# Optimization experiments

Measured on AMD Instinct MI355X. Metric: run time of the kernel, lower is better.

## Reference

```python
import jax, jax.numpy as jnp
import numpy as np

EMBED = 512
HEADS = 8
DIM_HEAD = 64          # embed_dim // 8
LANDMARKS = 256        # embed_dim // 2
PINV_ITERS = 6
RES_K = 33             # nystrom residual_conv_kernel default
SCALE = DIM_HEAD ** -0.5


def layer_norm(x, g, b, eps=1e-5):
    mu = x.mean(-1, keepdims=True)
    var = ((x - mu) ** 2).mean(-1, keepdims=True)
    return (x - mu) / jnp.sqrt(var + eps) * g + b


def moore_penrose_pinv(x, iters=PINV_ITERS):
    # iterative Moore-Penrose pseudo-inverse (lucidrains nystrom-attention)
    ax = jnp.abs(x)
    z = jnp.swapaxes(x, -1, -2) / (ax.sum(-1).max() * ax.sum(-2).max())
    I = jnp.eye(x.shape[-1], dtype=x.dtype)
    for _ in range(iters):
        xz = x @ z
        z = 0.25 * z @ (13. * I - xz @ (15. * I - xz @ (7. * I - xz)))
    return z


def nystrom_attention(x, w_qkv, w_out, b_out, res_k):
    b, n, _ = x.shape
    m = LANDMARKS
    pad = (m - n % m) % m
    xp = jnp.pad(x, ((0, 0), (pad, 0), (0, 0)))  # left-pad like F.pad(..., padding, 0)
    np_ = n + pad
    qkv = (xp @ w_qkv).reshape(b, np_, 3, HEADS, DIM_HEAD)
    q = qkv[:, :, 0].transpose(0, 2, 1, 3) * SCALE   # [b,h,np,dh]
    k = qkv[:, :, 1].transpose(0, 2, 1, 3)
    v = qkv[:, :, 2].transpose(0, 2, 1, 3)
    l = np_ // m
    q_l = q.reshape(b, HEADS, m, l, DIM_HEAD).mean(3)  # [b,h,m,dh]
    k_l = k.reshape(b, HEADS, m, l, DIM_HEAD).mean(3)
    attn1 = jax.nn.softmax(jnp.einsum('bhid,bhjd->bhij', q, k_l), -1)    # [b,h,np,m]
    attn2 = jax.nn.softmax(jnp.einsum('bhid,bhjd->bhij', q_l, k_l), -1)  # [b,h,m,m]
    attn3 = jax.nn.softmax(jnp.einsum('bhid,bhjd->bhij', q_l, k), -1)    # [b,h,m,np]
    out = (attn1 @ moore_penrose_pinv(attn2)) @ (attn3 @ v)              # [b,h,np,dh]
    # depthwise residual conv over the sequence dim, per head (shared across dh)
    v_c = v.transpose(0, 3, 1, 2).reshape(b * DIM_HEAD, HEADS, np_)
    res = jax.lax.conv_general_dilated(
        v_c, res_k[:, None, :], (1,), [(RES_K // 2, RES_K // 2)],
        dimension_numbers=('NCH', 'OIH', 'NCH'), feature_group_count=HEADS)
    out = out + res.reshape(b, DIM_HEAD, HEADS, np_).transpose(0, 2, 3, 1)
    out = out.transpose(0, 2, 1, 3).reshape(b, np_, HEADS * DIM_HEAD)
    out = out @ w_out + b_out
    return out[:, -n:]  # drop left padding


def dwconv2d(x, w, b, k):
    # x: [B,C,H,W], w: [C,1,k,k] depthwise
    y = jax.lax.conv_general_dilated(
        x, w, (1, 1), [(k // 2, k // 2)] * 2,
        dimension_numbers=('NCHW', 'OIHW', 'NCHW'), feature_group_count=x.shape[1])
    return y + b[None, :, None, None]


def ppeg(x, H, W, w7, b7, w5, b5, w3, b3):
    B, _, C = x.shape
    cls_tok, feat = x[:, :1], x[:, 1:]
    f = feat.transpose(0, 2, 1).reshape(B, C, H, W)
    y = f + dwconv2d(f, w7, b7, 7) + dwconv2d(f, w5, b5, 5) + dwconv2d(f, w3, b3, 3)
    y = y.reshape(B, C, H * W).transpose(0, 2, 1)
    return jnp.concatenate([cls_tok, y], axis=1)


def reference(h, w_fc1, b_fc1, cls_token,
              ln1_g, ln1_b, qkv1_w, out1_w, out1_b, res1_k,
              conv7_w, conv7_b, conv5_w, conv5_b, conv3_w, conv3_b,
              ln2_g, ln2_b, qkv2_w, out2_w, out2_b, res2_k,
              lnf_g, lnf_b):
    h = jax.nn.relu(h @ w_fc1 + b_fc1)                 # [B,N,512]
    B, N, C = h.shape
    _H = int(np.ceil(np.sqrt(N)))
    add = _H * _H - N
    h = jnp.concatenate([h, h[:, :add]], axis=1)       # square padding
    h = jnp.concatenate([jnp.broadcast_to(cls_token, (B, 1, C)), h], axis=1)
    h = h + nystrom_attention(layer_norm(h, ln1_g, ln1_b), qkv1_w, out1_w, out1_b, res1_k)
    h = ppeg(h, _H, _H, conv7_w, conv7_b, conv5_w, conv5_b, conv3_w, conv3_b)
    h = h + nystrom_attention(layer_norm(h, ln2_g, ln2_b), qkv2_w, out2_w, out2_b, res2_k)
    return layer_norm(h, lnf_g, lnf_b)[:, 0]           # [B,512]


def setup_inputs() -> dict:
    key = jax.random.key(0)
    ks = jax.random.split(key, 24)
    B, N, IN_DIM = 2, 4096, 1024
    w = lambda k, shape, s=0.02: jax.random.normal(k, shape, jnp.float32) * s
    z = lambda shape: jnp.zeros(shape, jnp.float32)
    o = lambda shape: jnp.ones(shape, jnp.float32)
    return {
        'h': jax.random.normal(ks[0], (B, N, IN_DIM), jnp.float32),
        'w_fc1': w(ks[1], (IN_DIM, EMBED)), 'b_fc1': z((EMBED,)),
        'cls_token': w(ks[2], (1, 1, EMBED)),
        'ln1_g': o((EMBED,)), 'ln1_b': z((EMBED,)),
        'qkv1_w': w(ks[3], (EMBED, 3 * HEADS * DIM_HEAD)),
        'out1_w': w(ks[4], (HEADS * DIM_HEAD, EMBED)), 'out1_b': z((EMBED,)),
        'res1_k': w(ks[5], (HEADS, RES_K), 0.1),
        'conv7_w': w(ks[6], (EMBED, 1, 7, 7), 0.05), 'conv7_b': z((EMBED,)),
        'conv5_w': w(ks[7], (EMBED, 1, 5, 5), 0.05), 'conv5_b': z((EMBED,)),
        'conv3_w': w(ks[8], (EMBED, 1, 3, 3), 0.05), 'conv3_b': z((EMBED,)),
        'ln2_g': o((EMBED,)), 'ln2_b': z((EMBED,)),
        'qkv2_w': w(ks[9], (EMBED, 3 * HEADS * DIM_HEAD)),
        'out2_w': w(ks[10], (HEADS * DIM_HEAD, EMBED)), 'out2_b': z((EMBED,)),
        'res2_k': w(ks[11], (HEADS, RES_K), 0.1),
        'lnf_g': o((EMBED,)), 'lnf_b': z((EMBED,)),
    }
```

## Files before the change

### kernel.cpp

```cpp
#include <hip/hip_runtime.h>
#include <hip/hip_bf16.h>

#define HEADS 8
#define DH 64
#define EMB 512
#define NP 4352
#define NTOK 4097
#define PADF 255
#define LM 256
#define SCALE 0.125f

typedef __attribute__((ext_vector_type(8))) short bf8;
typedef __attribute__((ext_vector_type(4))) float f4;
typedef __attribute__((ext_vector_type(8))) unsigned short us8;
typedef __attribute__((ext_vector_type(4))) unsigned short us4;
typedef unsigned short u16;

__device__ __forceinline__ u16 f2b(float f){
  union { float f; unsigned u; } x; x.f = f;
  unsigned r = x.u + 0x7fffu + ((x.u>>16)&1u);
  return (u16)(r>>16);
}
__device__ __forceinline__ float b2f(u16 h){
  union { unsigned u; float f; } x; x.u = ((unsigned)h)<<16;
  return x.f;
}

__device__ __forceinline__ void gload_lds(const u16* g, u16* l){
  __builtin_amdgcn_global_load_lds((const __attribute__((address_space(1))) void*)g,
                                   (__attribute__((address_space(3))) void*)l, 16, 0, 0);
}

#define WAITCNT(N) asm volatile("s_waitcnt vmcnt(" #N ")" ::: "memory")
#define SCHED_FENCE() __builtin_amdgcn_sched_barrier(0)
#define BARRIER() __builtin_amdgcn_s_barrier()

template<int MODE>
__global__ __launch_bounds__(256)
void k_g128(const u16* __restrict__ A, const u16* __restrict__ B,
            float* __restrict__ C, u16* __restrict__ C16,
            int K, int lda, int ldb, int ldc,
            long sAb, long sAh, long sBb, long sBh, long sCb, long sCh, int nh,
            float alpha, const float* __restrict__ bias, int relu, int rowoff,
            int nx, int ksplit)
{
  int z = blockIdx.z;
  const u16* Ab = A + (long)(z/nh)*sAb + (long)(z%nh)*sAh;
  const u16* Bb = B + (long)(z/nh)*sBb + (long)(z%nh)*sBh;
  long cb = (long)(z/nh)*sCb + (long)(z%nh)*sCh;
  int bx = blockIdx.x % nx, kc = blockIdx.x / nx;
  int m0 = blockIdx.y*128, n0 = bx*128;
  int klen = K/ksplit, kbeg = kc*klen, nch = klen/32;
  __shared__ u16 As[2][4096];
  __shared__ u16 Bs[2][4096];
  int tid=threadIdx.x, w=tid>>6, lane=tid&63, q=lane>>4, lr=lane&15;
  int wrow=(w>>1)*64, wcol=(w&1)*64;
  int srow = tid>>2, scol = (tid&3)*8;
  const u16* ga  = Ab + (long)(m0+srow)*lda + kbeg + scol;
  const u16* ga2 = Ab + (long)(m0+64+srow)*lda + kbeg + scol;
  const u16* gb  = Bb + (long)(n0+srow)*ldb + kbeg + scol;
  const u16* gb2 = Bb + (long)(n0+64+srow)*ldb + kbeg + scol;
  int lo = srow*32 + scol;
  f4 acc[4][4] = {};
  auto stage = [&](int r, int c){
    gload_lds(ga  + c*32, &As[r][lo]);
    gload_lds(ga2 + c*32, &As[r][2048+lo]);
    gload_lds(gb  + c*32, &Bs[r][lo]);
    gload_lds(gb2 + c*32, &Bs[r][2048+lo]);
  };
  auto compute = [&](int r){
    bf8 af[4], bfr[4];
    #pragma unroll
    for(int rr=0;rr<4;rr++) af[rr]  = *(const bf8*)&As[r][(wrow + rr*16 + lr)*32 + q*8];
    #pragma unroll
    for(int t=0;t<4;t++) bfr[t] = *(const bf8*)&Bs[r][(wcol + t*16 + lr)*32 + q*8];
    #pragma unroll
    for(int rr=0;rr<4;rr++)
      #pragma unroll
      for(int t=0;t<4;t++)
        acc[rr][t] = __builtin_amdgcn_mfma_f32_16x16x32_bf16(af[rr], bfr[t], acc[rr][t], 0,0,0);
  };
  stage(0,0);
  stage(1,1);
  for(int c=0;c<nch;c++){
    if(c+1<nch) WAITCNT(4); else WAITCNT(0);
    SCHED_FENCE();
    BARRIER();
    compute(c&1);
    SCHED_FENCE();
    BARRIER();
    SCHED_FENCE();
    if(c+2<nch) stage(c&1, c+2);
  }
  #pragma unroll
  for(int r=0;r<4;r++){
    #pragma unroll
    for(int t=0;t<4;t++){
      #pragma unroll
      for(int e=0;e<4;e++){
        int gm = m0 + wrow + r*16 + q*4 + e;
        int gn = n0 + wcol + t*16 + lr;
        float v = acc[r][t][e]*alpha;
        if(MODE==4){
          if(bias && kc==0) v += bias[gn];
          if(gm>=rowoff) atomicAdd(&C[cb + (long)(gm-rowoff)*ldc + gn], v);
        } else {
          if(bias) v += bias[gn];
          if(relu) v = fmaxf(v,0.f);
          if(MODE==0) C[cb + (long)gm*ldc + gn] = v;
          else if(MODE==2) C16[cb + (long)gm*ldc + gn] = f2b(v);
          else { if(gm>=rowoff) C[cb + (long)(gm-rowoff)*ldc + gn] += v; }
        }
      }
    }
  }
}

template<int MODE>
__global__ __launch_bounds__(256)
void k_g64(const u16* __restrict__ A, const u16* __restrict__ B,
           float* __restrict__ C, u16* __restrict__ C16,
           int K, int lda, int ldb, int ldc,
           long sAb, long sAh, long sBb, long sBh, long sCb, long sCh, int nh,
           float alpha, const float* __restrict__ bias, int rowoff, int moff,
           int nx, int ksplit)
{
  int z = blockIdx.z;
  const u16* Ab = A + (long)(z/nh)*sAb + (long)(z%nh)*sAh;
  const u16* Bb = B + (long)(z/nh)*sBb + (long)(z%nh)*sBh;
  long cb = (long)(z/nh)*sCb + (long)(z%nh)*sCh;
  int bx = blockIdx.x % nx, kc = blockIdx.x / nx;
  int m0 = blockIdx.y*64 + moff, n0 = bx*64;
  int klen = K/ksplit, kbeg = kc*klen, nch = klen/32;
  __shared__ u16 As[2][2048];
  __shared__ u16 Bs[2][2048];
  int tid=threadIdx.x, w=tid>>6, lane=tid&63, q=lane>>4, lr=lane&15;
  int srow = tid>>2, scol = (tid&3)*8;
  const u16* ga = Ab + (long)(m0+srow)*lda + kbeg + scol;
  const u16* gb = Bb + (long)(n0+srow)*ldb + kbeg + scol;
  int lo = srow*32 + scol;
  f4 acc[4] = {};
  auto stage = [&](int r, int c){
    gload_lds(ga + c*32, &As[r][lo]);
    gload_lds(gb + c*32, &Bs[r][lo]);
  };
  auto compute = [&](int r){
    bf8 af = *(const bf8*)&As[r][(w*16 + lr)*32 + q*8];
    #pragma unroll
    for(int t=0;t<4;t++){
      bf8 bfr = *(const bf8*)&Bs[r][(t*16 + lr)*32 + q*8];
      acc[t] = __builtin_amdgcn_mfma_f32_16x16x32_bf16(af, bfr, acc[t], 0,0,0);
    }
  };
  stage(0,0);
  stage(1,1);
  for(int c=0;c<nch;c++){
    if(c+1<nch) WAITCNT(2); else WAITCNT(0);
    SCHED_FENCE();
    BARRIER();
    compute(c&1);
    SCHED_FENCE();
    BARRIER();
    SCHED_FENCE();
    if(c+2<nch) stage(c&1, c+2);
  }
  #pragma unroll
  for(int t=0;t<4;t++){
    #pragma unroll
    for(int e=0;e<4;e++){
      int gm = m0 + w*16 + q*4 + e;
      int gn = n0 + t*16 + lr;
      float v = acc[t][e]*alpha;
      if(MODE==0) C[cb + (long)gm*ldc + gn] = v;
      else if(MODE==2) C16[cb + (long)gm*ldc + gn] = f2b(v);
      else if(MODE==3) atomicAdd(&C[cb + (long)gm*ldc + gn], v);
      else if(MODE==5){
        v += bias[gn];
        if(gm>=rowoff) C[cb + (long)(gm-rowoff)*ldc + gn] += v;
      }
    }
  }
}

__global__ __launch_bounds__(256)
void k_pg3(const u16* __restrict__ Ah, const u16* __restrict__ Al,
           const u16* __restrict__ Bh, const u16* __restrict__ Bl,
           u16* __restrict__ Oh, u16* __restrict__ Ol, float na, float nd,
           u16* __restrict__ TOh, u16* __restrict__ TOl, float ta, float td)
{
  long zo = (long)blockIdx.z*65536;
  int m0 = blockIdx.y*32, n0 = blockIdx.x*64;
  __shared__ u16 S[2][6144];
  int tid=threadIdx.x, w=tid>>6, lane=tid&63, q=lane>>4, lr=lane&15;
  int t2 = tid & 127;
  const u16* srcA = (tid<128 ? Ah : Al) + zo + (long)(m0 + (t2>>2))*256 + (t2&3)*8;
  const u16* srcBh = Bh + zo + (long)(n0 + (tid>>2))*256 + (tid&3)*8;
  const u16* srcBl = Bl + zo + (long)(n0 + (tid>>2))*256 + (tid&3)*8;
  f4 acc[2] = {};
  auto stage = [&](int r, int c){
    gload_lds(srcA  + c*32, &S[r][tid*8]);
    gload_lds(srcBh + c*32, &S[r][2048 + tid*8]);
    gload_lds(srcBl + c*32, &S[r][4096 + tid*8]);
  };
  int mrow = (w>>1)*16 + lr;
  auto compute = [&](int r){
    bf8 ah = *(const bf8*)&S[r][mrow*32 + q*8];
    bf8 al = *(const bf8*)&S[r][1024 + mrow*32 + q*8];
    #pragma unroll
    for(int t=0;t<2;t++){
      int nrow = (w&1)*32 + t*16 + lr;
      bf8 bh = *(const bf8*)&S[r][2048 + nrow*32 + q*8];
      bf8 bl = *(const bf8*)&S[r][4096 + nrow*32 + q*8];
      acc[t] = __builtin_amdgcn_mfma_f32_16x16x32_bf16(ah, bh, acc[t], 0,0,0);
      acc[t] = __builtin_amdgcn_mfma_f32_16x16x32_bf16(ah, bl, acc[t], 0,0,0);
      acc[t] = __builtin_amdgcn_mfma_f32_16x16x32_bf16(al, bh, acc[t], 0,0,0);
    }
  };
  stage(0,0);
  stage(1,1);
  for(int c=0;c<8;c++){
    if(c<7) WAITCNT(3); else WAITCNT(0);
    SCHED_FENCE();
    BARRIER();
    compute(c&1);
    SCHED_FENCE();
    BARRIER();
    SCHED_FENCE();
    if(c+2<8) stage(c&1, c+2);
  }
  #pragma unroll
  for(int t=0;t<2;t++){
    int gn = n0 + (w&1)*32 + t*16 + lr;
    if(Oh){
      #pragma unroll
      for(int r=0;r<4;r++){
        int gm = m0 + (w>>1)*16 + q*4 + r;
        float v = na*acc[t][r] + ((gm==gn)?nd:0.f);
        u16 h = f2b(v);
        long o = zo + (long)gm*256 + gn;
        Oh[o] = h; Ol[o] = f2b(v - b2f(h));
      }
    }
    if(TOh){
      us4 th, tl;
      #pragma unroll
      for(int r=0;r<4;r++){
        int gm = m0 + (w>>1)*16 + q*4 + r;
        float v = ta*acc[t][r] + ((gm==gn)?td:0.f);
        u16 h = f2b(v);
        th[r] = h; tl[r] = f2b(v - b2f(h));
      }
      long o = zo + (long)gn*256 + (m0 + (w>>1)*16 + q*4);
      *(us4*)&TOh[o] = th; *(us4*)&TOl[o] = tl;
    }
  }
}

__global__ __launch_bounds__(256)
void k_pg3b(const u16* __restrict__ Zh, const u16* __restrict__ Zl,
            const u16* __restrict__ Ph, const u16* __restrict__ Pl,
            const u16* __restrict__ Bh, const u16* __restrict__ Bl,
            u16* __restrict__ Ozh, u16* __restrict__ Ozl,
            u16* __restrict__ Oyh, u16* __restrict__ Oyl,
            u16* __restrict__ Tyh, u16* __restrict__ Tyl)
{
  long zo = (long)blockIdx.z*65536;
  int ysel = blockIdx.y>>3;
  int m0 = (blockIdx.y&7)*32, n0 = blockIdx.x*64;
  const u16* Ah = ysel ? Ph : Zh;
  const u16* Al = ysel ? Pl : Zl;
  __shared__ u16 S[2][6144];
  int tid=threadIdx.x, w=tid>>6, lane=tid&63, q=lane>>4, lr=lane&15;
  int t2 = tid & 127;
  const u16* srcA = (tid<128 ? Ah : Al) + zo + (long)(m0 + (t2>>2))*256 + (t2&3)*8;
  const u16* srcBh = Bh + zo + (long)(n0 + (tid>>2))*256 + (tid&3)*8;
  const u16* srcBl = Bl + zo + (long)(n0 + (tid>>2))*256 + (tid&3)*8;
  f4 acc[2] = {};
  auto stage = [&](int r, int c){
    gload_lds(srcA  + c*32, &S[r][tid*8]);
    gload_lds(srcBh + c*32, &S[r][2048 + tid*8]);
    gload_lds(srcBl + c*32, &S[r][4096 + tid*8]);
  };
  int mrow = (w>>1)*16 + lr;
  auto compute = [&](int r){
    bf8 ah = *(const bf8*)&S[r][mrow*32 + q*8];
    bf8 al = *(const bf8*)&S[r][1024 + mrow*32 + q*8];
    #pragma unroll
    for(int t=0;t<2;t++){
      int nrow = (w&1)*32 + t*16 + lr;
      bf8 bh = *(const bf8*)&S[r][2048 + nrow*32 + q*8];
      bf8 bl = *(const bf8*)&S[r][4096 + nrow*32 + q*8];
      acc[t] = __builtin_amdgcn_mfma_f32_16x16x32_bf16(ah, bh, acc[t], 0,0,0);
      acc[t] = __builtin_amdgcn_mfma_f32_16x16x32_bf16(ah, bl, acc[t], 0,0,0);
      acc[t] = __builtin_amdgcn_mfma_f32_16x16x32_bf16(al, bh, acc[t], 0,0,0);
    }
  };
  stage(0,0);
  stage(1,1);
  for(int c=0;c<8;c++){
    if(c<7) WAITCNT(3); else WAITCNT(0);
    SCHED_FENCE();
    BARRIER();
    compute(c&1);
    SCHED_FENCE();
    BARRIER();
    SCHED_FENCE();
    if(c+2<8) stage(c&1, c+2);
  }
  #pragma unroll
  for(int t=0;t<2;t++){
    int gn = n0 + (w&1)*32 + t*16 + lr;
    if(!ysel){
      #pragma unroll
      for(int r=0;r<4;r++){
        int gm = m0 + (w>>1)*16 + q*4 + r;
        float v = 0.25f*acc[t][r];
        u16 h = f2b(v);
        long o = zo + (long)gm*256 + gn;
        Ozh[o] = h; Ozl[o] = f2b(v - b2f(h));
      }
    } else {
      us4 th, tl;
      #pragma unroll
      for(int r=0;r<4;r++){
        int gm = m0 + (w>>1)*16 + q*4 + r;
        float v = 0.25f*acc[t][r];
        u16 h = f2b(v);
        long o = zo + (long)gm*256 + gn;
        Oyh[o] = h; Oyl[o] = f2b(v - b2f(h));
        float tv = -v + ((gm==gn)?7.f:0.f);
        u16 h2 = f2b(tv);
        th[r] = h2; tl[r] = f2b(tv - b2f(h2));
      }
      long o = zo + (long)gn*256 + (m0 + (w>>1)*16 + q*4);
      *(us4*)&Tyh[o] = th; *(us4*)&Tyl[o] = tl;
    }
  }
}

__global__ __launch_bounds__(256)
void k_att3(const u16* __restrict__ qkv16, const u16* __restrict__ ql,
            const u16* __restrict__ vT, float* __restrict__ partO,
            float* __restrict__ pm, float* __restrict__ pl)
{
  int kc = blockIdx.x, jt = blockIdx.y, z = blockIdx.z;
  int b = z>>3, h = z&7;
  __shared__ u16 SQ[64*64];
  __shared__ u16 SK[2][64*64];
  __shared__ u16 SV[2][64*64];
  __shared__ u16 SP[64*64];
  int tid=threadIdx.x, w=tid>>6, lane=tid&63, q=lane>>4, lr=lane&15;
  const u16* kb = qkv16 + (long)b*NP*1536 + 512 + h*64;
  const u16* vb = vT + (long)z*64*NP;
  int t00 = kc*256;
  {
    const u16* qb = ql + (long)z*16384 + jt*64*64;
    #pragma unroll
    for(int p=0;p<2;p++){
      int idx = tid + p*256; int row = idx>>3; int js = ((idx&7)^(row&7))<<3;
      gload_lds(qb + row*64 + js, &SQ[idx*8]);
    }
  }
  auto stageKV = [&](int r, int i){
    int t0 = t00 + i*64;
    #pragma unroll
    for(int p=0;p<2;p++){
      int idx = tid + p*256; int row = idx>>3; int js = ((idx&7)^(row&7))<<3;
      gload_lds(kb + (long)(t0+row)*1536 + js, &SK[r][idx*8]);
      gload_lds(vb + (long)row*NP + t0 + js, &SV[r][idx*8]);
    }
  };
  stageKV(0,0);
  __syncthreads();
  int ar = w*16+lr;
  bf8 af0 = *(const bf8*)&SQ[ar*64 + ((q^(ar&7))<<3)];
  bf8 af1 = *(const bf8*)&SQ[ar*64 + (((q|4)^(ar&7))<<3)];
  f4 o[4] = {};
  float m[4] = {-3e38f,-3e38f,-3e38f,-3e38f};
  float l[4] = {0.f,0.f,0.f,0.f};
  for(int i=0;i<4;i++){
    int cur = i&1;
    if(i<3) stageKV(cur^1, i+1);
    f4 s[4] = {};
    #pragma unroll
    for(int t=0;t<4;t++){
      int br = t*16+lr;
      bf8 b0 = *(const bf8*)&SK[cur][br*64 + ((q^(br&7))<<3)];
      bf8 b1 = *(const bf8*)&SK[cur][br*64 + (((q|4)^(br&7))<<3)];
      s[t] = __builtin_amdgcn_mfma_f32_16x16x32_bf16(af0, b0, s[t], 0,0,0);
      s[t] = __builtin_amdgcn_mfma_f32_16x16x32_bf16(af1, b1, s[t], 0,0,0);
    }
    float tm[4];
    #pragma unroll
    for(int e=0;e<4;e++) tm[e] = fmaxf(fmaxf(s[0][e],s[1][e]), fmaxf(s[2][e],s[3][e]));
    #pragma unroll
    for(int sh=1; sh<16; sh<<=1)
      #pragma unroll
      for(int e=0;e<4;e++) tm[e] = fmaxf(tm[e], __shfl_xor(tm[e], sh));
    float rs[4];
    #pragma unroll
    for(int e=0;e<4;e++){
      float mn = fmaxf(m[e], tm[e]);
      float sc = expf(m[e]-mn);
      m[e] = mn;
      l[e] *= sc;
      rs[e] = 0.f;
      o[0][e]*=sc; o[1][e]*=sc; o[2][e]*=sc; o[3][e]*=sc;
    }
    #pragma unroll
    for(int t=0;t<4;t++)
      #pragma unroll
      for(int e=0;e<4;e++){
        float p = expf(s[t][e]-m[e]);
        rs[e] += p;
        int prow = w*16+q*4+e, pcol = t*16+lr;
        SP[prow*64 + (((pcol>>3)^(prow&7))<<3) + (pcol&7)] = f2b(p);
      }
    #pragma unroll
    for(int sh=1; sh<16; sh<<=1)
      #pragma unroll
      for(int e=0;e<4;e++) rs[e] += __shfl_xor(rs[e], sh);
    #pragma unroll
    for(int e=0;e<4;e++) l[e] += rs[e];
    int pr = w*16+lr;
    #pragma unroll
    for(int ks=0;ks<2;ks++){
      bf8 pa = *(const bf8*)&SP[pr*64 + (((ks*4+q)^(pr&7))<<3)];
      #pragma unroll
      for(int t2=0;t2<4;t2++){
        int rr = t2*16+lr;
        bf8 vv = *(const bf8*)&SV[cur][rr*64 + (((ks*4+q)^(rr&7))<<3)];
        o[t2] = __builtin_amdgcn_mfma_f32_16x16x32_bf16(pa, vv, o[t2], 0,0,0);
      }
    }
    __syncthreads();
  }
  long pb = (long)(z*17+kc)*256 + jt*64 + w*16;
  #pragma unroll
  for(int e=0;e<4;e++){
    int jg = q*4+e;
    #pragma unroll
    for(int t2=0;t2<4;t2++)
      partO[(pb + jg)*64 + t2*16 + lr] = o[t2][e];
    if(lr==0){ pm[pb + jg] = m[e]; pl[pb + jg] = l[e]; }
  }
}

__global__ __launch_bounds__(128)
void k_mrg3(const float* __restrict__ partO, const float* __restrict__ pm,
            const float* __restrict__ pl, u16* __restrict__ avbT16)
{
  int jq = blockIdx.x, z = blockIdx.y, tid = threadIdx.x;
  int j0 = jq*16;
  __shared__ float wk[16][17];
  __shared__ u16 T[16][72];
  if(tid < 16){
    int j = j0 + tid;
    float mm[17];
    float M = -3e38f;
    #pragma unroll
    for(int kc=0;kc<17;kc++){ mm[kc]=pm[(z*17+kc)*256 + j]; M=fmaxf(M,mm[kc]); }
    float s = 0.f;
    #pragma unroll
    for(int kc=0;kc<17;kc++){ float e=expf(mm[kc]-M); wk[tid][kc]=e; s+=e*pl[(z*17+kc)*256 + j]; }
    float inv = 1.f/s;
    #pragma unroll
    for(int kc=0;kc<17;kc++) wk[tid][kc]*=inv;
  }
  __syncthreads();
  float acc[8];
  #pragma unroll
  for(int p=0;p<8;p++) acc[p]=0.f;
  for(int kc=0;kc<17;kc++){
    long base = ((long)(z*17+kc)*256 + j0)*64;
    #pragma unroll
    for(int p=0;p<8;p++){
      int idx = tid + p*128;
      acc[p] += wk[idx>>6][kc]*partO[base + idx];
    }
  }
  #pragma unroll
  for(int p=0;p<8;p++){ int idx = tid + p*128; T[idx>>6][idx&63] = f2b(acc[p]); }
  __syncthreads();
  int d = tid>>1, jh = (tid&1)*8;
  us8 vv;
  #pragma unroll
  for(int u=0;u<8;u++) vv[u] = T[jh+u][d];
  *(us8*)&avbT16[(long)(z*64+d)*256 + j0 + jh] = vv;
}

__global__ __launch_bounds__(256)
void k_att1(const u16* __restrict__ qkv16, const u16* __restrict__ kl,
            const u16* __restrict__ zavT, float* __restrict__ Qc)
{
  int z = blockIdx.y, b = z>>3, h = z&7;
  int m0 = blockIdx.x*64;
  __shared__ u16 SQ[64*64];
  __shared__ u16 SKL[256*64];
  __shared__ u16 SZV[64*256];
  int tid=threadIdx.x, w=tid>>6, lane=tid&63, q=lane>>4, lr=lane&15;
  {
    const u16* qb = qkv16 + (long)b*NP*1536 + h*64;
    #pragma unroll
    for(int p=0;p<2;p++){
      int idx = tid + p*256; int row = idx>>3; int js = ((idx&7)^(row&7))<<3;
      gload_lds(qb + (long)(m0+row)*1536 + js, &SQ[idx*8]);
    }
    const u16* kb = kl + (long)z*16384;
    #pragma unroll
    for(int p=0;p<8;p++){
      int idx = tid + p*256; int row = idx>>3; int js = ((idx&7)^(row&7))<<3;
      gload_lds(kb + row*64 + js, &SKL[idx*8]);
    }
    const u16* zb = zavT + (long)z*16384;
    #pragma unroll
    for(int p=0;p<8;p++){
      int idx = tid + p*256; int row = idx>>5; int cs = ((idx&31)^(row&7))<<3;
      gload_lds(zb + row*256 + cs, &SZV[idx*8]);
    }
  }
  __syncthreads();
  f4 acc[16] = {};
  {
    int ar = w*16+lr;
    bf8 af0 = *(const bf8*)&SQ[ar*64 + ((q^(ar&7))<<3)];
    bf8 af1 = *(const bf8*)&SQ[ar*64 + (((q|4)^(ar&7))<<3)];
    #pragma unroll
    for(int t=0;t<16;t++){
      int br = t*16+lr;
      bf8 b0 = *(const bf8*)&SKL[br*64 + ((q^(br&7))<<3)];
      bf8 b1 = *(const bf8*)&SKL[br*64 + (((q|4)^(br&7))<<3)];
      acc[t] = __builtin_amdgcn_mfma_f32_16x16x32_bf16(af0, b0, acc[t], 0,0,0);
      acc[t] = __builtin_amdgcn_mfma_f32_16x16x32_bf16(af1, b1, acc[t], 0,0,0);
    }
  }
  float mx[4] = {-1e30f,-1e30f,-1e30f,-1e30f};
  #pragma unroll
  for(int t=0;t<16;t++)
    #pragma unroll
    for(int e=0;e<4;e++) mx[e] = fmaxf(mx[e], acc[t][e]*SCALE);
  #pragma unroll
  for(int s=1;s<16;s<<=1)
    #pragma unroll
    for(int e=0;e<4;e++) mx[e] = fmaxf(mx[e], __shfl_xor(mx[e], s));
  float sm[4] = {0.f,0.f,0.f,0.f};
  #pragma unroll
  for(int t=0;t<16;t++)
    #pragma unroll
    for(int e=0;e<4;e++){ float p = expf(acc[t][e]*SCALE - mx[e]); acc[t][e]=p; sm[e]+=p; }
  #pragma unroll
  for(int s=1;s<16;s<<=1)
    #pragma unroll
    for(int e=0;e<4;e++) sm[e] += __shfl_xor(sm[e], s);
  float inv[4];
  #pragma unroll
  for(int e=0;e<4;e++) inv[e] = 1.f/sm[e];
  __syncthreads();
  u16* PS = SKL;
  #pragma unroll
  for(int t=0;t<16;t++)
    #pragma unroll
    for(int e=0;e<4;e++){
      int prow = w*16 + q*4 + e, pcol = t*16 + lr;
      PS[prow*256 + (((pcol>>3)^(prow&7))<<3) + (pcol&7)] = f2b(acc[t][e]*inv[e]);
    }
  __syncthreads();
  f4 acc2[4] = {};
  int pr = w*16+lr;
  #pragma unroll
  for(int ks=0;ks<8;ks++){
    bf8 af = *(const bf8*)&PS[pr*256 + (((ks*4+q)^(pr&7))<<3)];
    #pragma unroll
    for(int t=0;t<4;t++){
      int rr = t*16+lr;
      bf8 bf_ = *(const bf8*)&SZV[rr*256 + (((ks*4+q)^(rr&7))<<3)];
      acc2[t] = __builtin_amdgcn_mfma_f32_16x16x32_bf16(af, bf_, acc2[t], 0,0,0);
    }
  }
  #pragma unroll
  for(int t=0;t<4;t++)
    #pragma unroll
    for(int r=0;r<4;r++){
      int gm = m0 + w*16 + q*4 + r;
      int gd = t*16 + lr;
      Qc[((long)b*NP + gm)*512 + h*64 + gd] = acc2[t][r];
    }
}

__global__ __launch_bounds__(256)
void k_smw32(float* __restrict__ X){
  long row = (long)blockIdx.x*4 + (threadIdx.x>>6);
  int lane = threadIdx.x & 63;
  float* p = X + row*256;
  float4 v = *(float4*)&p[lane*4];
  float m = fmaxf(fmaxf(v.x,v.y),fmaxf(v.z,v.w));
  for(int s=32;s;s>>=1) m = fmaxf(m, __shfl_xor(m, s));
  float e0=expf(v.x-m), e1=expf(v.y-m), e2=expf(v.z-m), e3=expf(v.w-m);
  float sum = e0+e1+e2+e3;
  for(int s=32;s;s>>=1) sum += __shfl_xor(sum, s);
  float inv = 1.f/sum;
  float4 o = {e0*inv, e1*inv, e2*inv, e3*inv};
  *(float4*)&p[lane*4] = o;
}

__global__ void k_wT(const float* __restrict__ in, u16* __restrict__ out, int K, int N){
  int n0=blockIdx.x*32, k0=blockIdx.y*32, tid=threadIdx.x;
  __shared__ float T[32][33];
  int lr=tid&31, lc=tid>>5;
  #pragma unroll
  for(int p=0;p<4;p++) T[lc+8*p][lr] = in[(long)(k0+lc+8*p)*N + n0+lr];
  __syncthreads();
  #pragma unroll
  for(int p=0;p<4;p++) out[(long)(n0+lc+8*p)*K + k0+lr] = f2b(T[lr][lc+8*p]);
}

__global__ __launch_bounds__(256)
void k_vT(const u16* __restrict__ qkv16, u16* __restrict__ vT){
  int t0=blockIdx.x*64, h=blockIdx.y, b=blockIdx.z, tid=threadIdx.x;
  __shared__ u16 T[64][72];
  const u16* src = qkv16 + (long)b*NP*1536 + 1024 + h*64;
  for(int s=0;s<2;s++){
    int idx=tid+s*256; int row=idx>>3, c8=(idx&7)*8;
    *(us8*)&T[row][c8] = *(const us8*)&src[(long)(t0+row)*1536 + c8];
  }
  __syncthreads();
  u16* dst = vT + ((long)(b*8+h)*64)*NP;
  int d = tid>>2, j0=(tid&3)*16;
  us8 v0,v1;
  #pragma unroll
  for(int jj=0;jj<8;jj++){ v0[jj]=T[j0+jj][d]; v1[jj]=T[j0+8+jj][d]; }
  *(us8*)&dst[(long)d*NP + t0 + j0]     = v0;
  *(us8*)&dst[(long)d*NP + t0 + j0 + 8] = v1;
}

__global__ void k_cvt16(const float* __restrict__ in, u16* __restrict__ out, long n){
  long i = (long)blockIdx.x*256 + threadIdx.x;
  if(i<n) out[i] = f2b(in[i]);
}

__global__ void k_cls(const float* __restrict__ cls, float* __restrict__ seq){
  int b = blockIdx.x;
  seq[(long)b*NTOK*EMB + threadIdx.x] = cls[threadIdx.x];
}

__global__ void k_ln_pad(const float* __restrict__ seq, u16* __restrict__ xp,
                         const float* __restrict__ g, const float* __restrict__ bb){
  int b = blockIdx.y, i = blockIdx.x, tid = threadIdx.x;
  u16* out = xp + ((long)b*NP + i)*EMB;
  if(i < PADF){ out[tid]=0; out[tid+256]=0; return; }
  const float* x = seq + ((long)b*NTOK + (i-PADF))*EMB;
  float v0 = x[tid], v1 = x[tid+256];
  __shared__ float red[256];
  red[tid]=v0+v1; __syncthreads();
  for(int s=128;s>0;s>>=1){ if(tid<s) red[tid]+=red[tid+s]; __syncthreads(); }
  float mu = red[0]*(1.0f/512.0f); __syncthreads();
  float d0=v0-mu, d1=v1-mu;
  red[tid]=d0*d0+d1*d1; __syncthreads();
  for(int s=128;s>0;s>>=1){ if(tid<s) red[tid]+=red[tid+s]; __syncthreads(); }
  float rstd = rsqrtf(red[0]*(1.0f/512.0f) + 1e-5f);
  out[tid]     = f2b(d0*rstd*g[tid]     + bb[tid]);
  out[tid+256] = f2b(d1*rstd*g[tid+256] + bb[tid+256]);
}

__global__ void k_landmarks(const u16* __restrict__ qkv, u16* __restrict__ q_l, u16* __restrict__ k_l){
  int j = blockIdx.x*4 + (threadIdx.x>>6), h = blockIdx.y, b = blockIdx.z, d = threadIdx.x&63;
  const u16* base = qkv + (long)b*NP*1536 + h*64 + d;
  float sq=0.f, sk=0.f;
  for(int l=0;l<17;l++){
    long row = (long)(j*17+l)*1536;
    sq += b2f(base[row]);
    sk += b2f(base[row+512]);
  }
  long o = (((long)b*HEADS + h)*LM + j)*DH + d;
  q_l[o] = f2b(sq * (SCALE/17.0f));
  k_l[o] = f2b(sk * (1.0f/17.0f));
}

__global__ void k_pinv_norm(const float* __restrict__ A2, float* __restrict__ rmax, float* __restrict__ cmax){
  int z = blockIdx.x, tid = threadIdx.x;
  const float* X = A2 + (long)z*65536;
  float rs=0.f, cs=0.f;
  for(int j=0;j<256;j++){ rs += fabsf(X[tid*256+j]); cs += fabsf(X[j*256+tid]); }
  __shared__ float r1[256], r2[256];
  r1[tid]=rs; r2[tid]=cs; __syncthreads();
  for(int s=128;s>0;s>>=1){ if(tid<s){ r1[tid]=fmaxf(r1[tid],r1[tid+s]); r2[tid]=fmaxf(r2[tid],r2[tid+s]); } __syncthreads(); }
  if(tid==0){ rmax[z]=r1[0]; cmax[z]=r2[0]; }
}

__global__ void k_pair_init(const float* __restrict__ att2,
    const float* __restrict__ rmax, const float* __restrict__ cmax,
    u16* __restrict__ Xh, u16* __restrict__ Xl,
    u16* __restrict__ Zh, u16* __restrict__ Zl,
    u16* __restrict__ Zth, u16* __restrict__ Ztl)
{
  long zo = (long)blockIdx.z*65536;
  int i0 = blockIdx.y*64, j0 = blockIdx.x*64;
  float rm=0.f, cm=0.f;
  for(int t=0;t<16;t++){ rm=fmaxf(rm,rmax[t]); cm=fmaxf(cm,cmax[t]); }
  float inv = 1.0f/(rm*cm);
  __shared__ float T[64][68];
  int tid = threadIdx.x;
  int li = tid>>2, jc = (tid&3)*16;
  #pragma unroll
  for(int u=0;u<4;u++){
    float4 v = *(const float4*)&att2[zo + (long)(i0+li)*256 + j0 + jc + u*4];
    T[li][jc+u*4]=v.x; T[li][jc+u*4+1]=v.y; T[li][jc+u*4+2]=v.z; T[li][jc+u*4+3]=v.w;
    long o = zo + (long)(i0+li)*256 + j0 + jc + u*4;
    float vv[4] = {v.x,v.y,v.z,v.w};
    us4 xh, xl, zth, ztl;
    #pragma unroll
    for(int c=0;c<4;c++){
      u16 h = f2b(vv[c]); xh[c]=h; xl[c]=f2b(vv[c]-b2f(h));
      float zt = vv[c]*inv;
      u16 h2 = f2b(zt); zth[c]=h2; ztl[c]=f2b(zt-b2f(h2));
    }
    *(us4*)&Xh[o]=xh; *(us4*)&Xl[o]=xl; *(us4*)&Zth[o]=zth; *(us4*)&Ztl[o]=ztl;
  }
  __syncthreads();
  int lj = tid>>2, ic = (tid&3)*16;
  #pragma unroll
  for(int r=0;r<16;r++){
    float x = T[ic+r][lj]*inv;
    u16 h = f2b(x);
    long o = zo + (long)(j0+lj)*256 + i0 + ic + r;
    Zh[o]=h; Zl[o]=f2b(x-b2f(h));
  }
}

__global__ __launch_bounds__(256)
void k_rconv(const u16* __restrict__ qkv16, const float* __restrict__ resk,
             const float* __restrict__ Qin, u16* __restrict__ Qo16){
  int t0 = blockIdx.x*64, h = blockIdx.y, b = blockIdx.z;
  __shared__ float V[96*64];
  const u16* vb = qkv16 + (long)b*NP*1536 + 1024 + h*64;
  int tid = threadIdx.x;
  #pragma unroll
  for(int s=0;s<3;s++){
    int idx = tid + s*256;
    int row = idx>>3, c8 = (idx&7)*8;
    int p = t0 - 16 + row;
    if(p>=0 && p<NP){
      us8 v = *(const us8*)&vb[(long)p*1536 + c8];
      #pragma unroll
      for(int jj=0;jj<8;jj++) V[row*64+c8+jj] = b2f(v[jj]);
    } else {
      #pragma unroll
      for(int jj=0;jj<8;jj++) V[row*64+c8+jj] = 0.f;
    }
  }
  __syncthreads();
  int d = tid&63, lt = (tid>>6)*16;
  float acc[16] = {};
  #pragma unroll
  for(int s=0;s<48;s++){
    float val = V[(lt+s)*64 + d];
    #pragma unroll
    for(int j=0;j<16;j++){
      int tap = s - j;
      if(tap>=0 && tap<33) acc[j] += resk[h*33+tap]*val;
    }
  }
  #pragma unroll
  for(int j=0;j<16;j++){
    long idx = ((long)b*NP + t0 + lt + j)*EMB + h*64 + d;
    Qo16[idx] = f2b(Qin[idx] + acc[j]);
  }
}

__global__ __launch_bounds__(256)
void k_ppeg(const float* __restrict__ seq, float* __restrict__ out,
    const float* __restrict__ w7,const float* __restrict__ b7,
    const float* __restrict__ w5,const float* __restrict__ b5,
    const float* __restrict__ w3,const float* __restrict__ b3){
  int b = blockIdx.z, cg = blockIdx.y;
  int rp = blockIdx.x>>1, xs = blockIdx.x&1;
  int ch0 = cg*64;
  __shared__ float s7[64*49], s5[64*25], s3[64*9], sbias[64];
  int tid = threadIdx.x;
  for(int i=tid;i<64*49;i+=256) s7[i] = w7[ch0*49+i];
  for(int i=tid;i<64*25;i+=256) s5[i] = w5[ch0*25+i];
  for(int i=tid;i<64*9;i+=256)  s3[i] = w3[ch0*9+i];
  if(tid<64) sbias[tid] = b7[ch0+tid]+b5[ch0+tid]+b3[ch0+tid];
  if(cg==0 && blockIdx.x==0){
    out[(long)b*NTOK*EMB + tid]       = seq[(long)b*NTOK*EMB + tid];
    out[(long)b*NTOK*EMB + 256 + tid] = seq[(long)b*NTOK*EMB + 256 + tid];
  }
  __syncthreads();
  int c = tid & 63;
  int y = rp*4 + (tid>>6);
  const float* sbase = seq + (long)b*NTOK*EMB + EMB + (ch0 + c);
  float* obase = out + (long)b*NTOK*EMB + EMB + (ch0 + c);
  const float* W7 = &s7[c*49];
  const float* W5 = &s5[c*25];
  const float* W3 = &s3[c*9];
  float bsum = sbias[c];
  for(int xc=0;xc<4;xc++){
    int xb = xs*32 + xc*8;
    float acc[8];
    #pragma unroll
    for(int j=0;j<8;j++) acc[j] = sbase[(long)(y*64+xb+j)*EMB] + bsum;
    #pragma unroll
    for(int dy=-3;dy<=3;dy++){
      int yy = y+dy;
      if(yy<0||yy>=64) continue;
      float v[14];
      #pragma unroll
      for(int u=0;u<14;u++){
        int xx = xb + u - 3;
        v[u] = (xx>=0 && xx<64) ? sbase[(long)(yy*64+xx)*EMB] : 0.f;
      }
      #pragma unroll
      for(int dx=-3;dx<=3;dx++){
        float wsum = W7[(dy+3)*7+(dx+3)];
        if(dy>=-2&&dy<=2&&dx>=-2&&dx<=2) wsum += W5[(dy+2)*5+(dx+2)];
        if(dy>=-1&&dy<=1&&dx>=-1&&dx<=1) wsum += W3[(dy+1)*3+(dx+1)];
        #pragma unroll
        for(int j=0;j<8;j++) acc[j] += v[j+dx+3]*wsum;
      }
    }
    #pragma unroll
    for(int j=0;j<8;j++) obase[(long)(y*64+xb+j)*EMB] = acc[j];
  }
}

__global__ void k_final_ln(const float* __restrict__ seq, const float* __restrict__ g,
                           const float* __restrict__ bb, float* __restrict__ out){
  int b = blockIdx.x, tid = threadIdx.x;
  const float* x = seq + (long)b*NTOK*EMB;
  float v0 = x[tid], v1 = x[tid+256];
  __shared__ float red[256];
  red[tid]=v0+v1; __syncthreads();
  for(int s=128;s>0;s>>=1){ if(tid<s) red[tid]+=red[tid+s]; __syncthreads(); }
  float mu = red[0]*(1.0f/512.0f); __syncthreads();
  float d0=v0-mu, d1=v1-mu;
  red[tid]=d0*d0+d1*d1; __syncthreads();
  for(int s=128;s>0;s>>=1){ if(tid<s) red[tid]+=red[tid+s]; __syncthreads(); }
  float rstd = rsqrtf(red[0]*(1.0f/512.0f) + 1e-5f);
  out[b*512+tid]     = d0*rstd*g[tid]     + bb[tid];
  out[b*512+tid+256] = d1*rstd*g[tid+256] + bb[tid+256];
}

extern "C" void kernel_launch(void* const* d_in, const int* in_sizes, int n_in,
                              void* d_out, int out_size, void* d_ws, size_t ws_size,
                              hipStream_t stream) {
  const float* in[24];
  for(int i=0;i<24;i++) in[i] = (const float*)d_in[i];

  float* W = (float*)d_ws;
  size_t off = 0;
  float* seqA = W+off; off += 4195328;
  float* seqB = W+off; off += 4195328;
  float* att2 = W+off; off += 1048576;
  float* Qc   = W+off; off += 4456448;
  float* partO= W+off; off += 17825792;
  float* pm   = W+off; off += 69632;
  float* pl   = W+off; off += 69632;
  u16* xpb    = (u16*)(W+off); off += 2228224;
  u16* qkvb16 = (u16*)(W+off); off += 6684672;
  u16* vT16   = (u16*)(W+off); off += 2228224;
  u16* q_l16  = (u16*)(W+off); off += 131072;
  u16* k_l16  = (u16*)(W+off); off += 131072;
  u16* avbT16 = (u16*)(W+off); off += 131072;
  u16* zavT16 = (u16*)(W+off); off += 131072;
  u16* Qc16   = (u16*)(W+off); off += 2228224;
  u16* qkvwT1 = (u16*)(W+off); off += 393216;
  u16* qkvwT2 = (u16*)(W+off); off += 393216;
  u16* outwT1 = (u16*)(W+off); off += 131072;
  u16* outwT2 = (u16*)(W+off); off += 131072;
  u16* pairs  = (u16*)(W+off); off += 9437184;
  float* rmax = W+off; off += 16;
  float* cmax = W+off; off += 16;
  if (ws_size < off*sizeof(float)) return;

  u16* h16   = pairs;
  u16* wfc1T = pairs + 8388608;

  const long PB = 1048576;
  u16 *Xh=pairs,        *Xl=pairs+PB;
  u16 *Z0h=pairs+2*PB,  *Z0l=pairs+3*PB;
  u16 *Z0th=pairs+4*PB, *Z0tl=pairs+5*PB;
  u16 *Z1h=pairs+6*PB,  *Z1l=pairs+7*PB;
  u16 *P0h=pairs+8*PB,  *P0l=pairs+9*PB;
  u16 *P1h=pairs+10*PB, *P1l=pairs+11*PB;
  u16 *Tth=pairs+12*PB, *Ttl=pairs+13*PB;
  u16 *Uth=pairs+14*PB, *Utl=pairs+15*PB;
  u16 *Vth=pairs+16*PB, *Vtl=pairs+17*PB;

  k_cvt16<<<32768,256,0,stream>>>(in[0], h16, 8388608L);
  k_wT<<<dim3(16,32),256,0,stream>>>(in[1],  wfc1T, 1024, 512);
  k_wT<<<dim3(48,16),256,0,stream>>>(in[6],  qkvwT1, 512, 1536);
  k_wT<<<dim3(48,16),256,0,stream>>>(in[18], qkvwT2, 512, 1536);
  k_wT<<<dim3(16,16),256,0,stream>>>(in[7],  outwT1, 512, 512);
  k_wT<<<dim3(16,16),256,0,stream>>>(in[19], outwT2, 512, 512);

  k_g128<0><<<dim3(4,32,2),256,0,stream>>>(h16, wfc1T, seqA+EMB, nullptr,
      1024, 1024,1024,512, 4194304L,0, 0,0, (long)NTOK*EMB,0, 1, 1.0f, in[2], 1, 0, 4, 1);
  k_cls<<<2,512,0,stream>>>(in[3], seqA);

  auto attention = [&](float* seq, const float* lng,const float* lnb,
                       const u16* qkvwT, const u16* outwT, const float* outb, const float* resk){
    k_ln_pad<<<dim3(NP,2),256,0,stream>>>(seq, xpb, lng, lnb);
    k_g128<2><<<dim3(12,34,2),256,0,stream>>>(xpb, qkvwT, nullptr, qkvb16,
        512, 512,512,1536, (long)NP*512,0, 0,0, (long)NP*1536,0, 1, 1.0f, nullptr, 0, 0, 12, 1);
    k_landmarks<<<dim3(64,HEADS,2),256,0,stream>>>(qkvb16, q_l16, k_l16);
    k_vT<<<dim3(68,8,2),256,0,stream>>>(qkvb16, vT16);
    k_g128<0><<<dim3(2,2,16),256,0,stream>>>(q_l16, k_l16, att2, nullptr,
        64, 64,64,256, 0,16384, 0,16384, 0,65536, 16, 1.0f, nullptr, 0, 0, 2, 1);
    k_smw32<<<1024,256,0,stream>>>(att2);
    k_pinv_norm<<<16,256,0,stream>>>(att2, rmax, cmax);
    k_pair_init<<<dim3(4,4,16),256,0,stream>>>(att2, rmax, cmax, Xh,Xl, Z0h,Z0l, Z0th,Z0tl);
    dim3 pgrid(4,8,16);
    k_pg3<<<pgrid,256,0,stream>>>(Xh,Xl, Z0th,Z0tl, P0h,P0l,1.0f,0.f, Tth,Ttl,-1.0f,7.f);
    for(int it=0; it<6; it++){
      u16 *Zh_=(it&1)?Z1h:Z0h, *Zl_=(it&1)?Z1l:Z0l;
      u16 *Nh_=(it&1)?Z0h:Z1h, *Nl_=(it&1)?Z0l:Z1l;
      u16 *Pch=(it&1)?P1h:P0h, *Pcl=(it&1)?P1l:P0l;
      u16 *Pnh=(it&1)?P0h:P1h, *Pnl=(it&1)?P0l:P1l;
      k_pg3<<<pgrid,256,0,stream>>>(Pch,Pcl, Tth,Ttl, nullptr,nullptr,0.f,0.f, Uth,Utl,-1.0f,15.f);
      k_pg3<<<pgrid,256,0,stream>>>(Pch,Pcl, Uth,Utl, nullptr,nullptr,0.f,0.f, Vth,Vtl,-1.0f,13.f);
      if(it<5) k_pg3b<<<dim3(4,16,16),256,0,stream>>>(Zh_,Zl_, Pch,Pcl, Vth,Vtl,
                                                      Nh_,Nl_, Pnh,Pnl, Tth,Ttl);
      else     k_pg3<<<pgrid,256,0,stream>>>(Zh_,Zl_, Vth,Vtl, Nh_,Nl_,0.25f,0.f,
                                             nullptr,nullptr,0.f,0.f);
    }
    k_att3<<<dim3(17,4,16),256,0,stream>>>(qkvb16, q_l16, vT16, partO, pm, pl);
    k_mrg3<<<dim3(16,16),128,0,stream>>>(partO, pm, pl, avbT16);
    k_g64<2><<<dim3(4,1,16),256,0,stream>>>(avbT16, Z0h, nullptr, zavT16,
        256, 256,256,256, 0,16384L, 0,65536L, 0,16384L, 16, 1.0f, nullptr, 0, 0, 4, 1);
    k_att1<<<dim3(68,16),256,0,stream>>>(qkvb16, k_l16, zavT16, Qc);
    k_rconv<<<dim3(68,8,2),256,0,stream>>>(qkvb16, resk, Qc, Qc16);
    k_g64<5><<<dim3(8,65,2),256,0,stream>>>(Qc16, outwT, seq, nullptr,
        512, 512,512,512, (long)NP*512,0, 0,0, (long)NTOK*EMB,0, 1, 1.0f, outb, PADF, 192, 8, 1);
  };

  attention(seqA, in[4], in[5], qkvwT1, outwT1, in[8], in[9]);
  k_ppeg<<<dim3(32,8,2),256,0,stream>>>(seqA, seqB, in[10],in[11],in[12],in[13],in[14],in[15]);
  attention(seqB, in[16], in[17], qkvwT2, outwT2, in[20], in[21]);
  k_final_ln<<<2,256,0,stream>>>(seqB, in[22], in[23], (float*)d_out);
}
```

Baseline: 879.7 us.

## Triple-buffer GEMM LDS pipelines and fuse attn2 softmax with pinv norm

All MFMA GEMM kernels move from double- to triple-buffered LDS staging, with wait counts adjusted so more global loads are in flight. A new fused kernel computes q_l·k_l^T, applies the row softmax and accumulates column sums atomically. It replaces the separate GEMM, softmax and norm kernels, and uses the fact that softmax rows sum to one so the row-max factor is 1. The extra LDS per block may reduce occupancy, and the atomics make the column sums order-dependent.

```diff
diff --git a/kernel.cpp b/kernel.cpp
--- a/kernel.cpp
+++ b/kernel.cpp
@@ -51,8 +51,8 @@
   int bx = blockIdx.x % nx, kc = blockIdx.x / nx;
   int m0 = blockIdx.y*128, n0 = bx*128;
   int klen = K/ksplit, kbeg = kc*klen, nch = klen/32;
-  __shared__ u16 As[2][4096];
-  __shared__ u16 Bs[2][4096];
+  __shared__ u16 As[3][4096];
+  __shared__ u16 Bs[3][4096];
   int tid=threadIdx.x, w=tid>>6, lane=tid&63, q=lane>>4, lr=lane&15;
   int wrow=(w>>1)*64, wcol=(w&1)*64;
   int srow = tid>>2, scol = (tid&3)*8;
@@ -81,16 +81,20 @@
         acc[rr][t] = __builtin_amdgcn_mfma_f32_16x16x32_bf16(af[rr], bfr[t], acc[rr][t], 0,0,0);
   };
   stage(0,0);
-  stage(1,1);
+  if(nch>1) stage(1,1);
+  if(nch>2) stage(2,2);
+  int bufc = 0;
   for(int c=0;c<nch;c++){
-    if(c+1<nch) WAITCNT(4); else WAITCNT(0);
+    int rem = nch-1-c;
+    if(rem>=2) WAITCNT(8); else if(rem==1) WAITCNT(4); else WAITCNT(0);
     SCHED_FENCE();
     BARRIER();
-    compute(c&1);
+    compute(bufc);
     SCHED_FENCE();
     BARRIER();
     SCHED_FENCE();
-    if(c+2<nch) stage(c&1, c+2);
+    if(c+3<nch) stage(bufc, c+3);
+    bufc = (bufc+1==3)?0:bufc+1;
   }
   #pragma unroll
   for(int r=0;r<4;r++){
@@ -132,8 +136,8 @@
   int bx = blockIdx.x % nx, kc = blockIdx.x / nx;
   int m0 = blockIdx.y*64 + moff, n0 = bx*64;
   int klen = K/ksplit, kbeg = kc*klen, nch = klen/32;
-  __shared__ u16 As[2][2048];
-  __shared__ u16 Bs[2][2048];
+  __shared__ u16 As[3][2048];
+  __shared__ u16 Bs[3][2048];
   int tid=threadIdx.x, w=tid>>6, lane=tid&63, q=lane>>4, lr=lane&15;
   int srow = tid>>2, scol = (tid&3)*8;
   const u16* ga = Ab + (long)(m0+srow)*lda + kbeg + scol;
@@ -153,16 +157,20 @@
     }
   };
   stage(0,0);
-  stage(1,1);
+  if(nch>1) stage(1,1);
+  if(nch>2) stage(2,2);
+  int bufc = 0;
   for(int c=0;c<nch;c++){
-    if(c+1<nch) WAITCNT(2); else WAITCNT(0);
+    int rem = nch-1-c;
+    if(rem>=2) WAITCNT(4); else if(rem==1) WAITCNT(2); else WAITCNT(0);
     SCHED_FENCE();
     BARRIER();
-    compute(c&1);
+    compute(bufc);
     SCHED_FENCE();
     BARRIER();
     SCHED_FENCE();
-    if(c+2<nch) stage(c&1, c+2);
+    if(c+3<nch) stage(bufc, c+3);
+    bufc = (bufc+1==3)?0:bufc+1;
   }
   #pragma unroll
   for(int t=0;t<4;t++){
@@ -190,7 +198,7 @@
 {
   long zo = (long)blockIdx.z*65536;
   int m0 = blockIdx.y*32, n0 = blockIdx.x*64;
-  __shared__ u16 S[2][6144];
+  __shared__ u16 S[3][6144];
   int tid=threadIdx.x, w=tid>>6, lane=tid&63, q=lane>>4, lr=lane&15;
   int t2 = tid & 127;
   const u16* srcA = (tid<128 ? Ah : Al) + zo + (long)(m0 + (t2>>2))*256 + (t2&3)*8;
@@ -218,15 +226,19 @@
   };
   stage(0,0);
   stage(1,1);
+  stage(2,2);
+  int bufc = 0;
   for(int c=0;c<8;c++){
-    if(c<7) WAITCNT(3); else WAITCNT(0);
+    int rem = 7-c;
+    if(rem>=2) WAITCNT(6); else if(rem==1) WAITCNT(3); else WAITCNT(0);
     SCHED_FENCE();
     BARRIER();
-    compute(c&1);
+    compute(bufc);
     SCHED_FENCE();
     BARRIER();
     SCHED_FENCE();
-    if(c+2<8) stage(c&1, c+2);
+    if(c+3<8) stage(bufc, c+3);
+    bufc = (bufc+1==3)?0:bufc+1;
   }
   #pragma unroll
   for(int t=0;t<2;t++){
@@ -269,7 +281,7 @@
   int m0 = (blockIdx.y&7)*32, n0 = blockIdx.x*64;
   const u16* Ah = ysel ? Ph : Zh;
   const u16* Al = ysel ? Pl : Zl;
-  __shared__ u16 S[2][6144];
+  __shared__ u16 S[3][6144];
   int tid=threadIdx.x, w=tid>>6, lane=tid&63, q=lane>>4, lr=lane&15;
   int t2 = tid & 127;
   const u16* srcA = (tid<128 ? Ah : Al) + zo + (long)(m0 + (t2>>2))*256 + (t2&3)*8;
@@ -297,15 +309,19 @@
   };
   stage(0,0);
   stage(1,1);
+  stage(2,2);
+  int bufc = 0;
   for(int c=0;c<8;c++){
-    if(c<7) WAITCNT(3); else WAITCNT(0);
+    int rem = 7-c;
+    if(rem>=2) WAITCNT(6); else if(rem==1) WAITCNT(3); else WAITCNT(0);
     SCHED_FENCE();
     BARRIER();
-    compute(c&1);
+    compute(bufc);
     SCHED_FENCE();
     BARRIER();
     SCHED_FENCE();
-    if(c+2<8) stage(c&1, c+2);
+    if(c+3<8) stage(bufc, c+3);
+    bufc = (bufc+1==3)?0:bufc+1;
   }
   #pragma unroll
   for(int t=0;t<2;t++){
@@ -335,6 +351,81 @@
       long o = zo + (long)gn*256 + (m0 + (w>>1)*16 + q*4);
       *(us4*)&Tyh[o] = th; *(us4*)&Tyl[o] = tl;
     }
+  }
+}
+
+__global__ __launch_bounds__(256)
+void k_att2f(const u16* __restrict__ ql, const u16* __restrict__ kl,
+             float* __restrict__ att2, float* __restrict__ colsum)
+{
+  int z = blockIdx.y;
+  int m0 = blockIdx.x*64;
+  __shared__ u16 SQ[64*64];
+  __shared__ u16 SKL[256*64];
+  int tid=threadIdx.x, w=tid>>6, lane=tid&63, q=lane>>4, lr=lane&15;
+  {
+    const u16* qb = ql + (long)z*16384 + m0*64;
+    #pragma unroll
+    for(int p=0;p<2;p++){
+      int idx = tid + p*256; int row = idx>>3; int js = ((idx&7)^(row&7))<<3;
+      gload_lds(qb + row*64 + js, &SQ[idx*8]);
+    }
+    const u16* kb = kl + (long)z*16384;
+    #pragma unroll
+    for(int p=0;p<8;p++){
+      int idx = tid + p*256; int row = idx>>3; int js = ((idx&7)^(row&7))<<3;
+      gload_lds(kb + row*64 + js, &SKL[idx*8]);
+    }
+  }
+  __syncthreads();
+  f4 acc[16] = {};
+  {
+    int ar = w*16+lr;
+    bf8 af0 = *(const bf8*)&SQ[ar*64 + ((q^(ar&7))<<3)];
+    bf8 af1 = *(const bf8*)&SQ[ar*64 + (((q|4)^(ar&7))<<3)];
+    #pragma unroll
+    for(int t=0;t<16;t++){
+      int br = t*16+lr;
+      bf8 b0 = *(const bf8*)&SKL[br*64 + ((q^(br&7))<<3)];
+      bf8 b1 = *(const bf8*)&SKL[br*64 + (((q|4)^(br&7))<<3)];
+      acc[t] = __builtin_amdgcn_mfma_f32_16x16x32_bf16(af0, b0, acc[t], 0,0,0);
+      acc[t] = __builtin_amdgcn_mfma_f32_16x16x32_bf16(af1, b1, acc[t], 0,0,0);
+    }
+  }
+  float mx[4] = {-1e30f,-1e30f,-1e30f,-1e30f};
+  #pragma unroll
+  for(int t=0;t<16;t++)
+    #pragma unroll
+    for(int e=0;e<4;e++) mx[e] = fmaxf(mx[e], acc[t][e]);
+  #pragma unroll
+  for(int s=1;s<16;s<<=1)
+    #pragma unroll
+    for(int e=0;e<4;e++) mx[e] = fmaxf(mx[e], __shfl_xor(mx[e], s));
+  float sm[4] = {0.f,0.f,0.f,0.f};
+  #pragma unroll
+  for(int t=0;t<16;t++)
+    #pragma unroll
+    for(int e=0;e<4;e++){ float p = expf(acc[t][e] - mx[e]); acc[t][e]=p; sm[e]+=p; }
+  #pragma unroll
+  for(int s=1;s<16;s<<=1)
+    #pragma unroll
+    for(int e=0;e<4;e++) sm[e] += __shfl_xor(sm[e], s);
+  float inv[4];
+  #pragma unroll
+  for(int e=0;e<4;e++) inv[e] = 1.f/sm[e];
+  float* ab = att2 + (long)z*65536;
+  #pragma unroll
+  for(int t=0;t<16;t++){
+    float cs = 0.f;
+    #pragma unroll
+    for(int e=0;e<4;e++){
+      float p = acc[t][e]*inv[e];
+      ab[(long)(m0 + w*16 + q*4 + e)*256 + t*16 + lr] = p;
+      cs += p;
+    }
+    cs += __shfl_xor(cs, 16);
+    cs += __shfl_xor(cs, 32);
+    if(q==0) atomicAdd(&colsum[z*256 + t*16 + lr], cs);
   }
 }
 
@@ -587,22 +678,6 @@
     }
 }
 
-__global__ __launch_bounds__(256)
-void k_smw32(float* __restrict__ X){
-  long row = (long)blockIdx.x*4 + (threadIdx.x>>6);
-  int lane = threadIdx.x & 63;
-  float* p = X + row*256;
-  float4 v = *(float4*)&p[lane*4];
-  float m = fmaxf(fmaxf(v.x,v.y),fmaxf(v.z,v.w));
-  for(int s=32;s;s>>=1) m = fmaxf(m, __shfl_xor(m, s));
-  float e0=expf(v.x-m), e1=expf(v.y-m), e2=expf(v.z-m), e3=expf(v.w-m);
-  float sum = e0+e1+e2+e3;
-  for(int s=32;s;s>>=1) sum += __shfl_xor(sum, s);
-  float inv = 1.f/sum;
-  float4 o = {e0*inv, e1*inv, e2*inv, e3*inv};
-  *(float4*)&p[lane*4] = o;
-}
-
 __global__ void k_wT(const float* __restrict__ in, u16* __restrict__ out, int K, int N){
   int n0=blockIdx.x*32, k0=blockIdx.y*32, tid=threadIdx.x;
   __shared__ float T[32][33];
@@ -662,7 +737,9 @@
   out[tid+256] = f2b(d1*rstd*g[tid+256] + bb[tid+256]);
 }
 
-__global__ void k_landmarks(const u16* __restrict__ qkv, u16* __restrict__ q_l, u16* __restrict__ k_l){
+__global__ void k_landmarks(const u16* __restrict__ qkv, u16* __restrict__ q_l, u16* __restrict__ k_l,
+                            float* __restrict__ colsum){
+  if(blockIdx.y==0 && blockIdx.z==0 && blockIdx.x<16) colsum[blockIdx.x*256 + threadIdx.x] = 0.f;
   int j = blockIdx.x*4 + (threadIdx.x>>6), h = blockIdx.y, b = blockIdx.z, d = threadIdx.x&63;
   const u16* base = qkv + (long)b*NP*1536 + h*64 + d;
   float sq=0.f, sk=0.f;
@@ -676,30 +753,26 @@
   k_l[o] = f2b(sk * (1.0f/17.0f));
 }
 
-__global__ void k_pinv_norm(const float* __restrict__ A2, float* __restrict__ rmax, float* __restrict__ cmax){
-  int z = blockIdx.x, tid = threadIdx.x;
-  const float* X = A2 + (long)z*65536;
-  float rs=0.f, cs=0.f;
-  for(int j=0;j<256;j++){ rs += fabsf(X[tid*256+j]); cs += fabsf(X[j*256+tid]); }
-  __shared__ float r1[256], r2[256];
-  r1[tid]=rs; r2[tid]=cs; __syncthreads();
-  for(int s=128;s>0;s>>=1){ if(tid<s){ r1[tid]=fmaxf(r1[tid],r1[tid+s]); r2[tid]=fmaxf(r2[tid],r2[tid+s]); } __syncthreads(); }
-  if(tid==0){ rmax[z]=r1[0]; cmax[z]=r2[0]; }
-}
-
 __global__ void k_pair_init(const float* __restrict__ att2,
-    const float* __restrict__ rmax, const float* __restrict__ cmax,
+    const float* __restrict__ colsum,
     u16* __restrict__ Xh, u16* __restrict__ Xl,
     u16* __restrict__ Zh, u16* __restrict__ Zl,
     u16* __restrict__ Zth, u16* __restrict__ Ztl)
 {
   long zo = (long)blockIdx.z*65536;
   int i0 = blockIdx.y*64, j0 = blockIdx.x*64;
-  float rm=0.f, cm=0.f;
-  for(int t=0;t<16;t++){ rm=fmaxf(rm,rmax[t]); cm=fmaxf(cm,cmax[t]); }
-  float inv = 1.0f/(rm*cm);
+  int tid = threadIdx.x;
+  __shared__ float cred[256];
+  {
+    float cm = 0.f;
+    #pragma unroll
+    for(int i=0;i<16;i++) cm = fmaxf(cm, colsum[tid + i*256]);
+    cred[tid] = cm; __syncthreads();
+    for(int s=128;s>0;s>>=1){ if(tid<s) cred[tid]=fmaxf(cred[tid],cred[tid+s]); __syncthreads(); }
+  }
+  float inv = 1.0f/cred[0];
+  __syncthreads();
   __shared__ float T[64][68];
-  int tid = threadIdx.x;
   int li = tid>>2, jc = (tid&3)*16;
   #pragma unroll
   for(int u=0;u<4;u++){
@@ -868,8 +941,7 @@
   u16* outwT1 = (u16*)(W+off); off += 131072;
   u16* outwT2 = (u16*)(W+off); off += 131072;
   u16* pairs  = (u16*)(W+off); off += 9437184;
-  float* rmax = W+off; off += 16;
-  float* cmax = W+off; off += 16;
+  float* colsum = W+off; off += 4096;
   if (ws_size < off*sizeof(float)) return;
 
   u16* h16   = pairs;
@@ -902,13 +974,10 @@
     k_ln_pad<<<dim3(NP,2),256,0,stream>>>(seq, xpb, lng, lnb);
     k_g128<2><<<dim3(12,34,2),256,0,stream>>>(xpb, qkvwT, nullptr, qkvb16,
         512, 512,512,1536, (long)NP*512,0, 0,0, (long)NP*1536,0, 1, 1.0f, nullptr, 0, 0, 12, 1);
-    k_landmarks<<<dim3(64,HEADS,2),256,0,stream>>>(qkvb16, q_l16, k_l16);
+    k_landmarks<<<dim3(64,HEADS,2),256,0,stream>>>(qkvb16, q_l16, k_l16, colsum);
     k_vT<<<dim3(68,8,2),256,0,stream>>>(qkvb16, vT16);
-    k_g128<0><<<dim3(2,2,16),256,0,stream>>>(q_l16, k_l16, att2, nullptr,
-        64, 64,64,256, 0,16384, 0,16384, 0,65536, 16, 1.0f, nullptr, 0, 0, 2, 1);
-    k_smw32<<<1024,256,0,stream>>>(att2);
-    k_pinv_norm<<<16,256,0,stream>>>(att2, rmax, cmax);
-    k_pair_init<<<dim3(4,4,16),256,0,stream>>>(att2, rmax, cmax, Xh,Xl, Z0h,Z0l, Z0th,Z0tl);
+    k_att2f<<<dim3(4,16),256,0,stream>>>(q_l16, k_l16, att2, colsum);
+    k_pair_init<<<dim3(4,4,16),256,0,stream>>>(att2, colsum, Xh,Xl, Z0h,Z0l, Z0th,Z0tl);
     dim3 pgrid(4,8,16);
     k_pg3<<<pgrid,256,0,stream>>>(Xh,Xl, Z0th,Z0tl, P0h,P0l,1.0f,0.f, Tth,Ttl,-1.0f,7.f);
     for(int it=0; it<6; it++){
```

After: 850.1 us (median of 2 runs). 1.03x faster.
